# Kernel optimization log

Hardware: AMD Instinct MI355X
Metric: run time of the kernel (lower is better)

## Reference

```python
import jax, jax.numpy as jnp
import numpy as np

DIM = 192
HEADS = 6
HD = 56            # inverted head dim: int((DIM//HEADS) * 1.75)
WIN = 7
N = WIN * WIN      # 49 tokens per window
NW = 64            # windows per image (56x56 map, 7x7 windows)
B_ = 2048          # num_windows * batch
SCALE = (DIM // HEADS) ** (-0.5)  # scale uses ORIGINAL head_dim=32


def _rel_index():
    # same construction as the torch buffer relative_position_index
    coords = np.stack(np.meshgrid(np.arange(WIN), np.arange(WIN), indexing='ij'))
    flat = coords.reshape(2, -1)                      # (2, N)
    rel = flat[:, :, None] - flat[:, None, :]          # (2, N, N)
    rel = rel.transpose(1, 2, 0).astype(np.int64)      # (N, N, 2)
    rel[..., 0] += WIN - 1
    rel[..., 1] += WIN - 1
    rel[..., 0] *= 2 * WIN - 1
    return jnp.asarray(rel.sum(-1), dtype=jnp.int32)   # (N, N)


def setup_inputs() -> dict:
    key = jax.random.key(0)
    ks = jax.random.split(key, 6)
    qkv_out = HEADS * HD * 3  # 1008
    return {
        'x': jax.random.normal(ks[0], (B_, N, DIM), jnp.float32),
        'mask': jnp.zeros((NW, N, N), jnp.float32),
        'qkv_w': (jax.random.normal(ks[1], (DIM, qkv_out), jnp.float32) * 0.02),
        'qkv_b': jnp.zeros((qkv_out,), jnp.float32),
        'rel_bias_table': (jax.random.normal(ks[2], ((2 * WIN - 1) ** 2, HEADS), jnp.float32) * 0.02),
        'rel_index': _rel_index(),
        'lepe_w': (jax.random.normal(ks[3], (HEADS * HD, 1, 3, 3), jnp.float32) * 0.02),
        'lepe_b': jnp.zeros((HEADS * HD,), jnp.float32),
        'proj_w': (jax.random.normal(ks[4], (HEADS * HD, DIM), jnp.float32) * 0.02),
        'proj_b': jnp.zeros((DIM,), jnp.float32),
    }


def reference(x, mask, qkv_w, qkv_b, rel_bias_table, rel_index, lepe_w, lepe_b, proj_w, proj_b):
    B, n, C = x.shape
    # qkv projection: (B, N, 3*H*HD) -> (B, H, N, 3*HD)
    qkv = (x @ qkv_w + qkv_b).reshape(B, n, HEADS, 3 * HD).transpose(0, 2, 1, 3)
    q, k, v = qkv[..., :HD], qkv[..., HD:2 * HD], qkv[..., 2 * HD:]

    v_img = v.transpose(0, 1, 3, 2).reshape(B, HEADS * HD, WIN, WIN)
    lepe = jax.lax.conv_general_dilated(
        v_img, lepe_w, window_strides=(1, 1), padding='SAME',
        dimension_numbers=('NCHW', 'OIHW', 'NCHW'),
        feature_group_count=HEADS * HD) + lepe_b[None, :, None, None]
    lepe = lepe.reshape(B, HEADS * HD, n).transpose(0, 2, 1)  # (B, N, H*HD)

    # attention scores + relative position bias + mask
    attn = jnp.einsum('bhnd,bhmd->bhnm', q * SCALE, k)
    bias = rel_bias_table[rel_index.reshape(-1)].reshape(n, n, HEADS).transpose(2, 0, 1)
    attn = attn + bias[None]
    nW = mask.shape[0]
    attn = attn.reshape(B // nW, nW, HEADS, n, n) + mask[None, :, None]
    attn = jax.nn.softmax(attn.reshape(B, HEADS, n, n), axis=-1)

    out = jnp.einsum('bhnm,bhmd->bhnd', attn, v)
    out = out.transpose(0, 2, 1, 3).reshape(B, n, HEADS * HD) + lepe
    return out @ proj_w + proj_b
```

## Files before the change

kernel.cpp:

```cpp
#include <hip/hip_runtime.h>
#include <hip/hip_bf16.h>

typedef __bf16 bf16x8 __attribute__((ext_vector_type(8)));
typedef unsigned short u16x8 __attribute__((ext_vector_type(8)));
typedef float f32x4 __attribute__((ext_vector_type(4)));

#define NTOK 49
#define NH   6
#define HDIM 56
#define DIMC 192
#define SCALE 0.17677669529663687f

#define WS_QKVWT   0u
#define WS_PROJWT  387072u
#define WS_QKVBS   522240u
#define WS_BMALLT  526272u
#define WS_LEPET   3672000u
#define WS_QKV     3684288u
#define WS_NEED    (WS_QKV + (size_t)100352 * 2016 + 4096)
#define WS_XBF     (WS_QKV + (size_t)100352 * 2016)
#define WS_NEED2   (WS_XBF + (size_t)100352 * 384 + 4096)
#define FB_QKVWT  0
#define FB_PROJWT 387072
#define FB_BIAS6  534528

__device__ __forceinline__ unsigned swzaddr(unsigned base, int row, int colb, int strideb) {
  return base + (unsigned)((row * strideb + colb) ^ ((row & 7) << 4));
}

__device__ __forceinline__ unsigned short f2bu(float f) {
  __hip_bfloat16 h = __float2bfloat16(f);
  unsigned short u;
  __builtin_memcpy(&u, &h, 2);
  return u;
}

__device__ __forceinline__ float bu2f(unsigned short u) {
  union { unsigned int i; float f; } x;
  x.i = ((unsigned int)u) << 16;
  return x.f;
}


__global__ void prep_main(const float* __restrict__ qkv_w,
                          const float* __restrict__ qkv_b,
                          const float* __restrict__ proj_w,
                          const float* __restrict__ tbl,
                          const int* __restrict__ ridx,
                          const float* __restrict__ mask,
                          const float* __restrict__ lepe_w,
                          unsigned char* __restrict__ ws) {
  __hip_bfloat16* qkvwt   = (__hip_bfloat16*)(ws + WS_QKVWT);
  __hip_bfloat16* projwt2 = (__hip_bfloat16*)(ws + WS_PROJWT);
  float*          qkvbs   = (float*)(ws + WS_QKVBS);
  __hip_bfloat16* bmallT  = (__hip_bfloat16*)(ws + WS_BMALLT);
  float*          lepeT   = (float*)(ws + WS_LEPET);
  int idx = blockIdx.x * 256 + threadIdx.x;
  const int n1 = 1008 * 192;
  const int n2 = 192 * 352;
  const int n3 = 1008;
  const int n4 = 64 * 6 * 64 * 64;
  const int n5 = 9 * 336;
  if (idx < n1) {
    int c = idx / 192, k = idx - c * 192;
    float v = qkv_w[k * 1008 + c];
    if (c % 168 < 56) v *= SCALE;
    qkvwt[idx] = __float2bfloat16(v);
  } else if (idx < n1 + n2) {
    int j = idx - n1;
    int n = j / 352, kk = j - n * 352;
    projwt2[j] = __float2bfloat16(kk < 336 ? proj_w[kk * 192 + n] : 0.0f);
  } else if (idx < n1 + n2 + n3) {
    int c = idx - n1 - n2;
    float v = qkv_b[c];
    if (c % 168 < 56) v *= SCALE;
    qkvbs[c] = v;
  } else if (idx < n1 + n2 + n3 + n4) {
    int j = idx - n1 - n2 - n3;
    int wh = j >> 12;
    int e = j & 4095;
    int n = e >> 6, m = e & 63;
    int wdx = wh / 6, h = wh - wdx * 6;
    float v;
    if (n >= NTOK) v = -1e30f;
    else if (m >= NTOK) v = 0.0f;
    else v = tbl[ridx[m * NTOK + n] * NH + h] + mask[wdx * (NTOK * NTOK) + m * NTOK + n];
    bmallT[j] = __float2bfloat16(v);
  } else if (idx < n1 + n2 + n3 + n4 + n5) {
    int j = idx - n1 - n2 - n3 - n4;
    int tap = j / 336, hd = j - tap * 336;
    lepeT[j] = lepe_w[hd * 9 + tap];
  }
}

__global__ __launch_bounds__(256) void xcvt(const float* __restrict__ x,
                                            unsigned char* __restrict__ ws) {
  unsigned char* xbf = ws + WS_XBF;
  int i = blockIdx.x * 256 + threadIdx.x;
  if (i >= 2408448) return;
  const float4* p = (const float4*)(x + (size_t)i * 8);
  float4 a = p[0], b = p[1];
  union { unsigned short u[8]; uint4 q; } pk;
  pk.u[0] = f2bu(a.x); pk.u[1] = f2bu(a.y); pk.u[2] = f2bu(a.z); pk.u[3] = f2bu(a.w);
  pk.u[4] = f2bu(b.x); pk.u[5] = f2bu(b.y); pk.u[6] = f2bu(b.z); pk.u[7] = f2bu(b.w);
  *(uint4*)(xbf + (size_t)i * 16) = pk.q;
}

__global__ __launch_bounds__(256, 2) void qkv_gemm3(unsigned char* __restrict__ ws) {
  __shared__ uint4 smem4[2304];
  unsigned char* sm = (unsigned char*)smem4;
  const __hip_bfloat16* qkvwt = (const __hip_bfloat16*)(ws + WS_QKVWT);
  const float* qkvbs = (const float*)(ws + WS_QKVBS);
  const unsigned char* xbf = ws + WS_XBF;
  unsigned char* qkvbuf = ws + WS_QKV;

  const int tid = threadIdx.x;
  const int lane = tid & 63, wv = tid >> 6;
  const int l15 = lane & 15, l4 = lane >> 4;
  const int b = blockIdx.x;
  const int j = (b & 7) * 1372 + (b >> 3);
  const int nbase = (j % 7) * 144;
  const int mbase = (j / 7) * 64;

  f32x4 acc[9];
#pragma unroll
  for (int nt = 0; nt < 9; ++nt) {
    float bb = qkvbs[nbase + nt * 16 + l15];
    acc[nt] = (f32x4){bb, bb, bb, bb};
  }
  const unsigned char* xrow = xbf + (size_t)(mbase + wv * 16 + l15) * 384;

#pragma unroll
  for (int kh = 0; kh < 2; ++kh) {
    if (kh) __syncthreads();
    for (int jj = tid; jj < 1728; jj += 256) {
      int row = jj / 12, c16 = jj - row * 12;
      uint4 v = *(const uint4*)((const unsigned char*)qkvwt +
                                (size_t)(nbase + row) * 384 + kh * 192 + c16 * 16);
      *(uint4*)(sm + swzaddr(0, row, c16 * 16, 256)) = v;
    }
    bf16x8 afr[3];
#pragma unroll
    for (int kt2 = 0; kt2 < 3; ++kt2)
      afr[kt2] = *(const bf16x8*)(xrow + (kh * 3 + kt2) * 64 + l4 * 16);
    __syncthreads();
#pragma unroll
    for (int kt2 = 0; kt2 < 3; ++kt2) {
#pragma unroll
      for (int nt = 0; nt < 9; ++nt) {
        bf16x8 bf = *(const bf16x8*)(sm + swzaddr(0, nt * 16 + l15, kt2 * 64 + l4 * 16, 256));
        acc[nt] = __builtin_amdgcn_mfma_f32_16x16x32_bf16(afr[kt2], bf, acc[nt], 0, 0, 0);
      }
    }
  }
  __syncthreads();

#pragma unroll
  for (int nt = 0; nt < 9; ++nt)
#pragma unroll
    for (int r = 0; r < 4; ++r) {
      int row = wv * 16 + l4 * 4 + r;
      *(unsigned short*)(sm + swzaddr(0, row, (nt * 16 + l15) * 2, 320)) = f2bu(acc[nt][r]);
    }
  __syncthreads();
  for (int jj = tid; jj < 1152; jj += 256) {
    int row = jj / 18, c16 = jj - row * 18;
    uint4 v = *(const uint4*)(sm + swzaddr(0, row, c16 * 16, 320));
    *(uint4*)(qkvbuf + (size_t)(mbase + row) * 2016 + nbase * 2 + c16 * 16) = v;
  }
}

__global__ __launch_bounds__(256, 2) void qkv_gemm(
    const float* __restrict__ x, unsigned char* __restrict__ ws) {
  __shared__ uint4 smem4[2560];
  unsigned char* sm = (unsigned char*)smem4;
  const __hip_bfloat16* qkvwt = (const __hip_bfloat16*)(ws + WS_QKVWT);
  const float* qkvbs = (const float*)(ws + WS_QKVBS);
  unsigned char* qkvbuf = ws + WS_QKV;

  const int tid = threadIdx.x;
  const int lane = tid & 63, wv = tid >> 6;
  const int l15 = lane & 15, l4 = lane >> 4;
  const int b = blockIdx.x;
  const int j = (b & 7) * 686 + (b >> 3);
  const int nbase = (j % 7) * 144;
  const int mbase = (j / 7) * 128;

  bf16x8 afr[2][6];
#pragma unroll
  for (int mt = 0; mt < 2; ++mt) {
    int g = mbase + wv * 32 + mt * 16 + l15;
    const float* xr = x + (size_t)g * DIMC;
#pragma unroll
    for (int kt = 0; kt < 6; ++kt) {
      const float4* p = (const float4*)(xr + kt * 32 + l4 * 8);
      float4 a = p[0], bb = p[1];
      union { unsigned short u[8]; bf16x8 v; } pk;
      pk.u[0] = f2bu(a.x); pk.u[1] = f2bu(a.y); pk.u[2] = f2bu(a.z); pk.u[3] = f2bu(a.w);
      pk.u[4] = f2bu(bb.x); pk.u[5] = f2bu(bb.y); pk.u[6] = f2bu(bb.z); pk.u[7] = f2bu(bb.w);
      afr[mt][kt] = pk.v;
    }
  }

  f32x4 acc[2][9];
#pragma unroll
  for (int nt = 0; nt < 9; ++nt) {
    float bb = qkvbs[nbase + nt * 16 + l15];
    acc[0][nt] = (f32x4){bb, bb, bb, bb};
    acc[1][nt] = (f32x4){bb, bb, bb, bb};
  }

#pragma unroll
  for (int kh = 0; kh < 2; ++kh) {
    if (kh) __syncthreads();
    for (int jj = tid; jj < 1728; jj += 256) {
      int row = jj / 12, c16 = jj - row * 12;
      uint4 v = *(const uint4*)((const unsigned char*)qkvwt +
                                (size_t)(nbase + row) * 384 + kh * 192 + c16 * 16);
      *(uint4*)(sm + swzaddr(0, row, c16 * 16, 256)) = v;
    }
    __syncthreads();
#pragma unroll
    for (int kt2 = 0; kt2 < 3; ++kt2) {
      const int kt = kh * 3 + kt2;
#pragma unroll
      for (int nt = 0; nt < 9; ++nt) {
        bf16x8 bf = *(const bf16x8*)(sm + swzaddr(0, nt * 16 + l15, kt2 * 64 + l4 * 16, 256));
        acc[0][nt] = __builtin_amdgcn_mfma_f32_16x16x32_bf16(afr[0][kt], bf, acc[0][nt], 0, 0, 0);
        acc[1][nt] = __builtin_amdgcn_mfma_f32_16x16x32_bf16(afr[1][kt], bf, acc[1][nt], 0, 0, 0);
      }
    }
  }
  __syncthreads();

#pragma unroll
  for (int mt = 0; mt < 2; ++mt)
#pragma unroll
    for (int nt = 0; nt < 9; ++nt)
#pragma unroll
      for (int r = 0; r < 4; ++r) {
        int row = wv * 32 + mt * 16 + l4 * 4 + r;
        *(unsigned short*)(sm + swzaddr(0, row, (nt * 16 + l15) * 2, 320)) =
            f2bu(acc[mt][nt][r]);
      }
  __syncthreads();
  for (int jj = tid; jj < 2304; jj += 256) {
    int row = jj / 18, c16 = jj - row * 18;
    uint4 v = *(const uint4*)(sm + swzaddr(0, row, c16 * 16, 320));
    *(uint4*)(qkvbuf + (size_t)(mbase + row) * 2016 + nbase * 2 + c16 * 16) = v;
  }
}

#define A_KS   0u
#define A_VT   8192u
#define A_BMT  16384u
#define A_ATT  24576u
#define A_VS   32768u
#define A_SMEM 40960u

__global__ __launch_bounds__(256, 4) void attn_head(
    const float* __restrict__ lepe_b, unsigned char* __restrict__ ws) {
  __shared__ uint4 smem4[A_SMEM / 16];
  unsigned char* sm = (unsigned char*)smem4;
  const unsigned char* bmallT = ws + WS_BMALLT;
  const float* lepeT = (const float*)(ws + WS_LEPET);
  unsigned char* qkvbuf = ws + WS_QKV;

  const int tid = threadIdx.x;
  const int lane = tid & 63, wv = tid >> 6;
  const int l15 = lane & 15, l4 = lane >> 4;
  const int b = blockIdx.x;
  const int j = (b & 7) * 1536 + (b >> 3);
  const int h = j % 6;
  const int win = j / 6;
  const int wdx = win & 63;
  unsigned char* qbase = qkvbuf + (size_t)win * (NTOK * 2016);

  {
    uint4 z = {0u, 0u, 0u, 0u};
    for (int i = tid; i < 1024; i += 256) smem4[i] = z;
  }
  __syncthreads();

  for (int jj = tid; jj < 343; jj += 256) {
    int m = jj % 49, c = jj / 49;
    const unsigned char* row = qbase + (size_t)m * 2016 + h * 336;
    uint4 kv = *(const uint4*)(row + 112 + c * 16);
    *(uint4*)(sm + swzaddr(A_KS, m, c * 16, 128)) = kv;
    uint4 vv = *(const uint4*)(row + 224 + c * 16);
    *(uint4*)(sm + swzaddr(A_VS, m, c * 16, 128)) = vv;
    union { uint4 q; unsigned short u[8]; } pk; pk.q = vv;
#pragma unroll
    for (int e = 0; e < 8; ++e)
      *(unsigned short*)(sm + swzaddr(A_VT, c * 8 + e, m * 2, 128)) = pk.u[e];
  }
  {
    const uint4* src = (const uint4*)(bmallT + (size_t)(wdx * NH + h) * 8192);
    for (int jj = tid; jj < 512; jj += 256) {
      int n = jj >> 3, c = jj & 7;
      *(uint4*)(sm + swzaddr(A_BMT, n, c * 16, 128)) = src[jj];
    }
  }
  const int arow = wv * 16 + l15;
  const int xr = arow < NTOK ? arow : NTOK - 1;
  bf16x8 qa[2];
#pragma unroll
  for (int kt = 0; kt < 2; ++kt)
    qa[kt] = *(const bf16x8*)(qbase + (size_t)xr * 2016 + h * 336 + kt * 64 + l4 * 16);
  __syncthreads();

  const int mc0 = wv * 16 + l4 * 4;
  f32x4 sv[4];
#pragma unroll
  for (int nt = 0; nt < 4; ++nt) {
    int n = nt * 16 + l15;
    unsigned long long bm8 =
        *(const unsigned long long*)(sm + swzaddr(A_BMT, n, mc0 * 2, 128));
#pragma unroll
    for (int r = 0; r < 4; ++r)
      sv[nt][r] = bu2f((unsigned short)(bm8 >> (16 * r)));
#pragma unroll
    for (int kt = 0; kt < 2; ++kt) {
      bf16x8 kb = *(const bf16x8*)(sm + swzaddr(A_KS, n, kt * 64 + l4 * 16, 128));
      sv[nt] = __builtin_amdgcn_mfma_f32_16x16x32_bf16(qa[kt], kb, sv[nt], 0, 0, 0);
    }
  }

#pragma unroll
  for (int r = 0; r < 4; ++r) {
    float mx = fmaxf(fmaxf(sv[0][r], sv[1][r]), fmaxf(sv[2][r], sv[3][r]));
    mx = fmaxf(mx, __shfl_xor(mx, 1));
    mx = fmaxf(mx, __shfl_xor(mx, 2));
    mx = fmaxf(mx, __shfl_xor(mx, 4));
    mx = fmaxf(mx, __shfl_xor(mx, 8));
    float p0 = __expf(sv[0][r] - mx), p1 = __expf(sv[1][r] - mx);
    float p2 = __expf(sv[2][r] - mx), p3 = __expf(sv[3][r] - mx);
    float sum = p0 + p1 + p2 + p3;
    sum += __shfl_xor(sum, 1);
    sum += __shfl_xor(sum, 2);
    sum += __shfl_xor(sum, 4);
    sum += __shfl_xor(sum, 8);
    float rinv = 1.0f / sum;
    sv[0][r] = p0 * rinv; sv[1][r] = p1 * rinv; sv[2][r] = p2 * rinv; sv[3][r] = p3 * rinv;
  }
#pragma unroll
  for (int nt = 0; nt < 4; ++nt) {
    int n = nt * 16 + l15;
#pragma unroll
    for (int r = 0; r < 4; ++r) {
      int m = mc0 + r;
      if (m < NTOK)
        *(__hip_bfloat16*)(sm + swzaddr(A_ATT, m, n * 2, 128)) = __float2bfloat16(sv[nt][r]);
    }
  }

  bf16x8 pa[2];
#pragma unroll
  for (int kt = 0; kt < 2; ++kt)
    pa[kt] = *(const bf16x8*)(sm + swzaddr(A_ATT, arow, kt * 64 + l4 * 16, 128));
  f32x4 ov[4];
#pragma unroll
  for (int nt = 0; nt < 4; ++nt) {
    f32x4 a0 = (f32x4){0.f, 0.f, 0.f, 0.f};
#pragma unroll
    for (int kt = 0; kt < 2; ++kt) {
      bf16x8 vb = *(const bf16x8*)(sm + swzaddr(A_VT, nt * 16 + l15, kt * 64 + l4 * 16, 128));
      a0 = __builtin_amdgcn_mfma_f32_16x16x32_bf16(pa[kt], vb, a0, 0, 0, 0);
    }
    ov[nt] = a0;
  }

  __syncthreads();
#pragma unroll
  for (int nt = 0; nt < 4; ++nt) {
    int d = nt * 16 + l15;
#pragma unroll
    for (int r = 0; r < 4; ++r) {
      int m = mc0 + r;
      *(float*)(sm + swzaddr(0, m, d * 4, 256)) = ov[nt][r];
    }
  }
  __syncthreads();

  for (int jj = tid; jj < 343; jj += 256) {
    int m = jj % 49, c = jj / 49;
    int y = m / 7, x0 = m - y * 7;
    float4 o0 = *(const float4*)(sm + swzaddr(0, m, c * 32, 256));
    float4 o1 = *(const float4*)(sm + swzaddr(0, m, c * 32 + 16, 256));
    const float4* lb = (const float4*)(lepe_b + h * HDIM + c * 8);
    float4 b0 = lb[0], b1 = lb[1];
    float4 a0, a1;
    a0.x = o0.x + b0.x; a0.y = o0.y + b0.y; a0.z = o0.z + b0.z; a0.w = o0.w + b0.w;
    a1.x = o1.x + b1.x; a1.y = o1.y + b1.y; a1.z = o1.z + b1.z; a1.w = o1.w + b1.w;
#pragma unroll
    for (int dy = 0; dy < 3; ++dy) {
      int yy = y + dy - 1;
      if (yy < 0 || yy >= 7) continue;
#pragma unroll
      for (int dx = 0; dx < 3; ++dx) {
        int xx = x0 + dx - 1;
        if (xx < 0 || xx >= 7) continue;
        int mp = yy * 7 + xx;
        u16x8 vsv = *(const u16x8*)(sm + swzaddr(A_VS, mp, c * 16, 128));
        const float4* wr = (const float4*)(lepeT + (dy * 3 + dx) * 336 + h * HDIM + c * 8);
        float4 w0 = wr[0], w1 = wr[1];
        a0.x += w0.x * bu2f(vsv[0]); a0.y += w0.y * bu2f(vsv[1]);
        a0.z += w0.z * bu2f(vsv[2]); a0.w += w0.w * bu2f(vsv[3]);
        a1.x += w1.x * bu2f(vsv[4]); a1.y += w1.y * bu2f(vsv[5]);
        a1.z += w1.z * bu2f(vsv[6]); a1.w += w1.w * bu2f(vsv[7]);
      }
    }
    union { unsigned short u[8]; uint4 q; } st;
    st.u[0] = f2bu(a0.x); st.u[1] = f2bu(a0.y); st.u[2] = f2bu(a0.z); st.u[3] = f2bu(a0.w);
    st.u[4] = f2bu(a1.x); st.u[5] = f2bu(a1.y); st.u[6] = f2bu(a1.z); st.u[7] = f2bu(a1.w);
    *(uint4*)(qbase + (size_t)m * 2016 + h * 336 + c * 16) = st.q;
  }
}

__global__ __launch_bounds__(256, 3) void proj_gemm(
    const float* __restrict__ proj_b, unsigned char* __restrict__ ws,
    float* __restrict__ out) {
  __shared__ uint4 smem4[2816];
  unsigned char* sm = (unsigned char*)smem4;
  const unsigned char* projwt2 = ws + WS_PROJWT;
  const unsigned char* qkvbuf = ws + WS_QKV;

  const int tid = threadIdx.x;
  const int lane = tid & 63, wv = tid >> 6;
  const int l15 = lane & 15, l4 = lane >> 4;
  const int b = blockIdx.x;
  const int j = (b & 7) * 294 + (b >> 3);
  const int nbase = (j % 3) * 64;
  const int mbase = (j / 3) * 128;

  for (int jj = tid; jj < 2816; jj += 256) {
    int n = jj / 44, c = jj - n * 44;
    uint4 v = *(const uint4*)(projwt2 + (size_t)(nbase + n) * 704 + c * 16);
    *(uint4*)(sm + swzaddr(0, n, c * 16, 704)) = v;
  }
  f32x4 acc[2][4];
#pragma unroll
  for (int nt = 0; nt < 4; ++nt) {
    float bb = proj_b[nbase + nt * 16 + l15];
    acc[0][nt] = (f32x4){bb, bb, bb, bb};
    acc[1][nt] = (f32x4){bb, bb, bb, bb};
  }
  __syncthreads();

  for (int kt = 0; kt < 11; ++kt) {
    int ks = kt * 32 + l4 * 8;
    int hh = ks / 56;
    int rem = ks - hh * 56;
    unsigned aoff = (unsigned)(hh * 336 + rem * 2);
    bf16x8 af[2];
#pragma unroll
    for (int mt = 0; mt < 2; ++mt) {
      int row = mbase + wv * 32 + mt * 16 + l15;
      af[mt] = *(const bf16x8*)(qkvbuf + (size_t)row * 2016 + aoff);
    }
#pragma unroll
    for (int nt = 0; nt < 4; ++nt) {
      bf16x8 pb = *(const bf16x8*)(sm + swzaddr(0, nt * 16 + l15, (kt * 32 + l4 * 8) * 2, 704));
      acc[0][nt] = __builtin_amdgcn_mfma_f32_16x16x32_bf16(af[0], pb, acc[0][nt], 0, 0, 0);
      acc[1][nt] = __builtin_amdgcn_mfma_f32_16x16x32_bf16(af[1], pb, acc[1][nt], 0, 0, 0);
    }
  }
  __syncthreads();

#pragma unroll
  for (int mt = 0; mt < 2; ++mt)
#pragma unroll
    for (int nt = 0; nt < 4; ++nt)
#pragma unroll
      for (int r = 0; r < 4; ++r) {
        int m = wv * 32 + mt * 16 + l4 * 4 + r;
        *(float*)(sm + swzaddr(0, m, (nt * 16 + l15) * 4, 256)) = acc[mt][nt][r];
      }
  __syncthreads();
  for (int jj = tid; jj < 2048; jj += 256) {
    int row = jj >> 4, c = jj & 15;
    uint4 v = *(const uint4*)(sm + swzaddr(0, row, c * 16, 256));
    *(uint4*)((unsigned char*)out + (size_t)(mbase + row) * 768 + nbase * 4 + c * 16) = v;
  }
}


__global__ void prep_fb(const float* __restrict__ qkv_w,
                        const float* __restrict__ proj_w,
                        const float* __restrict__ tbl,
                        const int* __restrict__ ridx,
                        unsigned char* __restrict__ ws) {
  __hip_bfloat16* qkvwt  = (__hip_bfloat16*)(ws + FB_QKVWT);
  __hip_bfloat16* projwt = (__hip_bfloat16*)(ws + FB_PROJWT);
  float* bias6 = (float*)(ws + FB_BIAS6);
  int idx = blockIdx.x * 256 + threadIdx.x;
  const int n1 = 1008 * 192;
  const int n2 = 192 * 384;
  const int n3 = 6 * 49 * 49;
  if (idx < n1) {
    int c = idx / 192, k = idx - c * 192;
    qkvwt[idx] = __float2bfloat16(qkv_w[k * 1008 + c]);
  } else if (idx < n1 + n2) {
    int j = idx - n1;
    int c = j / 384, kk = j - c * 384;
    projwt[j] = __float2bfloat16(kk < 336 ? proj_w[kk * 192 + c] : 0.0f);
  } else if (idx < n1 + n2 + n3) {
    int j = idx - n1 - n2;
    int h = j / 2401, mn = j - h * 2401;
    bias6[j] = tbl[ridx[mn] * 6 + h];
  }
}

#define QS_OFF  0
#define KS_OFF  8192
#define VT_OFF  16384
#define ATT_OFF 24576
#define SMEM_BYTES 32768

__global__ __launch_bounds__(256, 4) void winattn_fb(
    const float* __restrict__ x, const float* __restrict__ mask,
    const float* __restrict__ qkv_b, const float* __restrict__ lepe_w,
    const float* __restrict__ lepe_b, const float* __restrict__ proj_b,
    const unsigned char* __restrict__ ws, float* __restrict__ out) {
  __shared__ uint4 smem4[SMEM_BYTES / 16];
  unsigned char* sm = (unsigned char*)smem4;
  const __hip_bfloat16* qkvwt  = (const __hip_bfloat16*)(ws + FB_QKVWT);
  const __hip_bfloat16* projwt = (const __hip_bfloat16*)(ws + FB_PROJWT);
  const float* bias6 = (const float*)(ws + FB_BIAS6);

  const int tid = threadIdx.x;
  const int lane = tid & 63, wv = tid >> 6;
  const int l15 = lane & 15, l4 = lane >> 4;
  const int blk = blockIdx.x;
  const int wdx = blk & 63;
  {
    uint4 z = {0u, 0u, 0u, 0u};
    for (int i = tid; i < SMEM_BYTES / 16; i += 256) smem4[i] = z;
  }
  const int arow = wv * 16 + l15;
  const float* xg = x + (size_t)blk * (NTOK * DIMC);
  const int xr = arow < NTOK ? arow : NTOK - 1;
  bf16x8 afr[6];
#pragma unroll
  for (int kt = 0; kt < 6; ++kt) {
    const float4* p = (const float4*)(xg + xr * DIMC + kt * 32 + l4 * 8);
    float4 a = p[0], b = p[1];
    union { unsigned short u[8]; bf16x8 v; } pk;
    pk.u[0] = f2bu(a.x); pk.u[1] = f2bu(a.y); pk.u[2] = f2bu(a.z); pk.u[3] = f2bu(a.w);
    pk.u[4] = f2bu(b.x); pk.u[5] = f2bu(b.y); pk.u[6] = f2bu(b.z); pk.u[7] = f2bu(b.w);
    afr[kt] = pk.v;
  }
  f32x4 pacc[12];
#pragma unroll
  for (int nt = 0; nt < 12; ++nt) {
    float pb = proj_b[nt * 16 + l15];
    pacc[nt] = (f32x4){pb, pb, pb, pb};
  }
  const float* maskw = mask + wdx * (NTOK * NTOK);
  __syncthreads();

  for (int h = 0; h < NH; ++h) {
    for (int i = tid; i < NTOK * NTOK; i += 256) {
      int row = i / NTOK, col = i - row * NTOK;
      *(unsigned short*)(sm + ATT_OFF + row * 128 + col * 2) =
          f2bu(bias6[h * (NTOK * NTOK) + i] + maskw[i]);
    }
#pragma unroll
    for (int nt = 0; nt < 11; ++nt) {
      int cl = nt * 16 + l15;
      int cg = h * 168 + cl; if (cg > 1007) cg = 1007;
      float bias = qkv_b[cg];
      f32x4 acc = (f32x4){bias, bias, bias, bias};
#pragma unroll
      for (int kt = 0; kt < 6; ++kt) {
        bf16x8 bf = *(const bf16x8*)(qkvwt + cg * DIMC + kt * 32 + l4 * 8);
        acc = __builtin_amdgcn_mfma_f32_16x16x32_bf16(afr[kt], bf, acc, 0, 0, 0);
      }
      if (cl < 168) {
#pragma unroll
        for (int r = 0; r < 4; ++r) {
          int m = wv * 16 + l4 * 4 + r;
          if (m < NTOK) {
            float vv = acc[r];
            if (cl < 56)
              *(__hip_bfloat16*)(sm + swzaddr(QS_OFF, m, cl * 2, 128)) = __float2bfloat16(vv);
            else if (cl < 112)
              *(__hip_bfloat16*)(sm + swzaddr(KS_OFF, m, (cl - 56) * 2, 128)) = __float2bfloat16(vv);
            else
              *(__hip_bfloat16*)(sm + swzaddr(VT_OFF, cl - 112, m * 2, 128)) = __float2bfloat16(vv);
          }
        }
      }
    }
    __syncthreads();
    bf16x8 qa[2];
#pragma unroll
    for (int kt = 0; kt < 2; ++kt)
      qa[kt] = *(const bf16x8*)(sm + swzaddr(QS_OFF, arow, (kt * 32 + l4 * 8) * 2, 128));
    f32x4 sv[4];
#pragma unroll
    for (int nt = 0; nt < 4; ++nt) {
      f32x4 acc = (f32x4){0.f, 0.f, 0.f, 0.f};
#pragma unroll
      for (int kt = 0; kt < 2; ++kt) {
        bf16x8 kb = *(const bf16x8*)(sm + swzaddr(KS_OFF, nt * 16 + l15, (kt * 32 + l4 * 8) * 2, 128));
        acc = __builtin_amdgcn_mfma_f32_16x16x32_bf16(qa[kt], kb, acc, 0, 0, 0);
      }
      sv[nt] = acc;
    }
#pragma unroll
    for (int nt = 0; nt < 4; ++nt) {
      int n = nt * 16 + l15;
#pragma unroll
      for (int r = 0; r < 4; ++r) {
        int m = wv * 16 + l4 * 4 + r;
        int mc = m < NTOK ? m : NTOK - 1;
        float vv;
        if (n < NTOK) {
          float add = __bfloat162float(
              *(const __hip_bfloat16*)(sm + ATT_OFF + mc * 128 + n * 2));
          vv = SCALE * sv[nt][r] + add;
        } else {
          vv = -1e30f;
        }
        sv[nt][r] = vv;
      }
    }
#pragma unroll
    for (int r = 0; r < 4; ++r) {
      float mx = fmaxf(fmaxf(sv[0][r], sv[1][r]), fmaxf(sv[2][r], sv[3][r]));
      mx = fmaxf(mx, __shfl_xor(mx, 1));
      mx = fmaxf(mx, __shfl_xor(mx, 2));
      mx = fmaxf(mx, __shfl_xor(mx, 4));
      mx = fmaxf(mx, __shfl_xor(mx, 8));
      float p0 = __expf(sv[0][r] - mx), p1 = __expf(sv[1][r] - mx);
      float p2 = __expf(sv[2][r] - mx), p3 = __expf(sv[3][r] - mx);
      float sum = p0 + p1 + p2 + p3;
      sum += __shfl_xor(sum, 1);
      sum += __shfl_xor(sum, 2);
      sum += __shfl_xor(sum, 4);
      sum += __shfl_xor(sum, 8);
      float rinv = 1.0f / sum;
      sv[0][r] = p0 * rinv; sv[1][r] = p1 * rinv; sv[2][r] = p2 * rinv; sv[3][r] = p3 * rinv;
    }
#pragma unroll
    for (int nt = 0; nt < 4; ++nt) {
      int n = nt * 16 + l15;
#pragma unroll
      for (int r = 0; r < 4; ++r) {
        int m = wv * 16 + l4 * 4 + r;
        if (m < NTOK)
          *(__hip_bfloat16*)(sm + swzaddr(ATT_OFF, m, n * 2, 128)) = __float2bfloat16(sv[nt][r]);
      }
    }
    bf16x8 pa[2];
#pragma unroll
    for (int kt = 0; kt < 2; ++kt)
      pa[kt] = *(const bf16x8*)(sm + swzaddr(ATT_OFF, arow, (kt * 32 + l4 * 8) * 2, 128));
    f32x4 ov[4];
#pragma unroll
    for (int nt = 0; nt < 4; ++nt) {
      f32x4 acc = (f32x4){0.f, 0.f, 0.f, 0.f};
#pragma unroll
      for (int kt = 0; kt < 2; ++kt) {
        bf16x8 vb = *(const bf16x8*)(sm + swzaddr(VT_OFF, nt * 16 + l15, (kt * 32 + l4 * 8) * 2, 128));
        acc = __builtin_amdgcn_mfma_f32_16x16x32_bf16(pa[kt], vb, acc, 0, 0, 0);
      }
      ov[nt] = acc;
    }
#pragma unroll
    for (int nt = 0; nt < 4; ++nt) {
      int d = nt * 16 + l15;
      if (d < HDIM) {
        const float* lw = lepe_w + (h * HDIM + d) * 9;
        float w9[9];
#pragma unroll
        for (int t9 = 0; t9 < 9; ++t9) w9[t9] = lw[t9];
        float lb = lepe_b[h * HDIM + d];
#pragma unroll
        for (int r = 0; r < 4; ++r) {
          int m = wv * 16 + l4 * 4 + r;
          if (m < NTOK) {
            int y = m / 7, x0 = m - y * 7;
            float lac = lb;
#pragma unroll
            for (int dy = 0; dy < 3; ++dy)
#pragma unroll
              for (int dx = 0; dx < 3; ++dx) {
                int yy = y + dy - 1, xx = x0 + dx - 1;
                if (yy >= 0 && yy < 7 && xx >= 0 && xx < 7) {
                  float vvv = __bfloat162float(
                      *(const __hip_bfloat16*)(sm + swzaddr(VT_OFF, d, (yy * 7 + xx) * 2, 128)));
                  lac += w9[dy * 3 + dx] * vvv;
                }
              }
            *(__hip_bfloat16*)(sm + swzaddr(QS_OFF, m, d * 2, 128)) =
                __float2bfloat16(ov[nt][r] + lac);
          }
        }
      }
    }
    bf16x8 oa[2];
#pragma unroll
    for (int kt = 0; kt < 2; ++kt)
      oa[kt] = *(const bf16x8*)(sm + swzaddr(QS_OFF, arow, (kt * 32 + l4 * 8) * 2, 128));
#pragma unroll
    for (int nt = 0; nt < 12; ++nt) {
#pragma unroll
      for (int kt = 0; kt < 2; ++kt) {
        bf16x8 pb = *(const bf16x8*)(projwt + (nt * 16 + l15) * 384 + h * HDIM + kt * 32 + l4 * 8);
        pacc[nt] = __builtin_amdgcn_mfma_f32_16x16x32_bf16(oa[kt], pb, pacc[nt], 0, 0, 0);
      }
    }
    __syncthreads();
  }
  float* og = out + (size_t)blk * (NTOK * DIMC);
#pragma unroll
  for (int nt = 0; nt < 12; ++nt) {
#pragma unroll
    for (int r = 0; r < 4; ++r) {
      int m = wv * 16 + l4 * 4 + r;
      if (m < NTOK) og[m * DIMC + nt * 16 + l15] = pacc[nt][r];
    }
  }
}


extern "C" void kernel_launch(void* const* d_in, const int* in_sizes, int n_in,
                              void* d_out, int out_size, void* d_ws, size_t ws_size,
                              hipStream_t stream) {
  const float* x      = (const float*)d_in[0];
  const float* mask   = (const float*)d_in[1];
  const float* qkv_w  = (const float*)d_in[2];
  const float* qkv_b  = (const float*)d_in[3];
  const float* tbl    = (const float*)d_in[4];
  const int*   ridx   = (const int*)d_in[5];
  const float* lepe_w = (const float*)d_in[6];
  const float* lepe_b = (const float*)d_in[7];
  const float* proj_w = (const float*)d_in[8];
  const float* proj_b = (const float*)d_in[9];
  unsigned char* ws = (unsigned char*)d_ws;
  float* out = (float*)d_out;

  if (ws_size >= WS_NEED) {
    const int n_prep = 1008 * 192 + 192 * 352 + 1008 + 64 * 6 * 64 * 64 + 9 * 336;
    prep_main<<<dim3((n_prep + 255) / 256), dim3(256), 0, stream>>>(
        qkv_w, qkv_b, proj_w, tbl, ridx, mask, lepe_w, ws);
    if (ws_size >= WS_NEED2) {
      xcvt<<<dim3(9408), dim3(256), 0, stream>>>(x, ws);
      qkv_gemm3<<<dim3(10976), dim3(256), 0, stream>>>(ws);
    } else {
      qkv_gemm<<<dim3(5488), dim3(256), 0, stream>>>(x, ws);
    }
    attn_head<<<dim3(12288), dim3(256), 0, stream>>>(lepe_b, ws);
    proj_gemm<<<dim3(2352), dim3(256), 0, stream>>>(proj_b, ws, out);
  } else {
    prep_fb<<<dim3(1101), dim3(256), 0, stream>>>(qkv_w, proj_w, tbl, ridx, ws);
    winattn_fb<<<dim3(2048), dim3(256), 0, stream>>>(x, mask, qkv_b, lepe_w, lepe_b,
                                                     proj_b, ws, out);
  }
}
```

Baseline: 296.3 us.

## Shrink attn_head LDS footprint, load bias to registers, store V as fp32

The bias/mask tile is now read straight from global memory into registers, and Q is loaded before the LDS zero-fill so both loads are in flight early. The attention-probability tile now reuses the K region after an added barrier, so the separate bias and prob LDS regions go away. LDS per block drops from 40 KB to 32 KB, which may allow more resident blocks. V for LePE is converted to fp32 once at staging so the 3x3 conv avoids repeated bf16 unpacking, at the cost of twice the LDS bytes per V read. It also uses a hardware reciprocal for the softmax normaliser.

```diff
diff --git a/kernel.cpp b/kernel.cpp
--- a/kernel.cpp
+++ b/kernel.cpp
@@ -253,10 +253,8 @@
 
 #define A_KS   0u
 #define A_VT   8192u
-#define A_BMT  16384u
-#define A_ATT  24576u
-#define A_VS   32768u
-#define A_SMEM 40960u
+#define A_VS   16384u
+#define A_SMEM 32768u
 
 __global__ __launch_bounds__(256, 4) void attn_head(
     const float* __restrict__ lepe_b, unsigned char* __restrict__ ws) {
@@ -276,6 +274,22 @@
   const int wdx = win & 63;
   unsigned char* qbase = qkvbuf + (size_t)win * (NTOK * 2016);
 
+  const int arow = wv * 16 + l15;
+  const int xr = arow < NTOK ? arow : NTOK - 1;
+  const int mc0 = wv * 16 + l4 * 4;
+
+  bf16x8 qa[2];
+#pragma unroll
+  for (int kt = 0; kt < 2; ++kt)
+    qa[kt] = *(const bf16x8*)(qbase + (size_t)xr * 2016 + h * 336 + kt * 64 + l4 * 16);
+  unsigned long long bm8[4];
+  {
+    const unsigned char* bmrow = bmallT + (size_t)(wdx * NH + h) * 8192;
+#pragma unroll
+    for (int nt = 0; nt < 4; ++nt)
+      bm8[nt] = *(const unsigned long long*)(bmrow + (nt * 16 + l15) * 128 + mc0 * 2);
+  }
+
   {
     uint4 z = {0u, 0u, 0u, 0u};
     for (int i = tid; i < 1024; i += 256) smem4[i] = z;
@@ -288,37 +302,25 @@
     uint4 kv = *(const uint4*)(row + 112 + c * 16);
     *(uint4*)(sm + swzaddr(A_KS, m, c * 16, 128)) = kv;
     uint4 vv = *(const uint4*)(row + 224 + c * 16);
-    *(uint4*)(sm + swzaddr(A_VS, m, c * 16, 128)) = vv;
     union { uint4 q; unsigned short u[8]; } pk; pk.q = vv;
 #pragma unroll
     for (int e = 0; e < 8; ++e)
       *(unsigned short*)(sm + swzaddr(A_VT, c * 8 + e, m * 2, 128)) = pk.u[e];
-  }
-  {
-    const uint4* src = (const uint4*)(bmallT + (size_t)(wdx * NH + h) * 8192);
-    for (int jj = tid; jj < 512; jj += 256) {
-      int n = jj >> 3, c = jj & 7;
-      *(uint4*)(sm + swzaddr(A_BMT, n, c * 16, 128)) = src[jj];
-    }
-  }
-  const int arow = wv * 16 + l15;
-  const int xr = arow < NTOK ? arow : NTOK - 1;
-  bf16x8 qa[2];
-#pragma unroll
-  for (int kt = 0; kt < 2; ++kt)
-    qa[kt] = *(const bf16x8*)(qbase + (size_t)xr * 2016 + h * 336 + kt * 64 + l4 * 16);
-  __syncthreads();
-
-  const int mc0 = wv * 16 + l4 * 4;
+    float4 vf0, vf1;
+    vf0.x = bu2f(pk.u[0]); vf0.y = bu2f(pk.u[1]); vf0.z = bu2f(pk.u[2]); vf0.w = bu2f(pk.u[3]);
+    vf1.x = bu2f(pk.u[4]); vf1.y = bu2f(pk.u[5]); vf1.z = bu2f(pk.u[6]); vf1.w = bu2f(pk.u[7]);
+    *(float4*)(sm + swzaddr(A_VS, m, c * 32, 256)) = vf0;
+    *(float4*)(sm + swzaddr(A_VS, m, c * 32 + 16, 256)) = vf1;
+  }
+  __syncthreads();
+
   f32x4 sv[4];
 #pragma unroll
   for (int nt = 0; nt < 4; ++nt) {
+#pragma unroll
+    for (int r = 0; r < 4; ++r)
+      sv[nt][r] = bu2f((unsigned short)(bm8[nt] >> (16 * r)));
     int n = nt * 16 + l15;
-    unsigned long long bm8 =
-        *(const unsigned long long*)(sm + swzaddr(A_BMT, n, mc0 * 2, 128));
-#pragma unroll
-    for (int r = 0; r < 4; ++r)
-      sv[nt][r] = bu2f((unsigned short)(bm8 >> (16 * r)));
 #pragma unroll
     for (int kt = 0; kt < 2; ++kt) {
       bf16x8 kb = *(const bf16x8*)(sm + swzaddr(A_KS, n, kt * 64 + l4 * 16, 128));
@@ -340,9 +342,11 @@
     sum += __shfl_xor(sum, 2);
     sum += __shfl_xor(sum, 4);
     sum += __shfl_xor(sum, 8);
-    float rinv = 1.0f / sum;
+    float rinv = __builtin_amdgcn_rcpf(sum);
     sv[0][r] = p0 * rinv; sv[1][r] = p1 * rinv; sv[2][r] = p2 * rinv; sv[3][r] = p3 * rinv;
   }
+
+  __syncthreads();
 #pragma unroll
   for (int nt = 0; nt < 4; ++nt) {
     int n = nt * 16 + l15;
@@ -350,14 +354,14 @@
     for (int r = 0; r < 4; ++r) {
       int m = mc0 + r;
       if (m < NTOK)
-        *(__hip_bfloat16*)(sm + swzaddr(A_ATT, m, n * 2, 128)) = __float2bfloat16(sv[nt][r]);
+        *(__hip_bfloat16*)(sm + swzaddr(A_KS, m, n * 2, 128)) = __float2bfloat16(sv[nt][r]);
     }
   }
 
   bf16x8 pa[2];
 #pragma unroll
   for (int kt = 0; kt < 2; ++kt)
-    pa[kt] = *(const bf16x8*)(sm + swzaddr(A_ATT, arow, kt * 64 + l4 * 16, 128));
+    pa[kt] = *(const bf16x8*)(sm + swzaddr(A_KS, arow, kt * 64 + l4 * 16, 128));
   f32x4 ov[4];
 #pragma unroll
   for (int nt = 0; nt < 4; ++nt) {
@@ -385,13 +389,12 @@
   for (int jj = tid; jj < 343; jj += 256) {
     int m = jj % 49, c = jj / 49;
     int y = m / 7, x0 = m - y * 7;
-    float4 o0 = *(const float4*)(sm + swzaddr(0, m, c * 32, 256));
-    float4 o1 = *(const float4*)(sm + swzaddr(0, m, c * 32 + 16, 256));
+    float4 a0 = *(const float4*)(sm + swzaddr(0, m, c * 32, 256));
+    float4 a1 = *(const float4*)(sm + swzaddr(0, m, c * 32 + 16, 256));
     const float4* lb = (const float4*)(lepe_b + h * HDIM + c * 8);
     float4 b0 = lb[0], b1 = lb[1];
-    float4 a0, a1;
-    a0.x = o0.x + b0.x; a0.y = o0.y + b0.y; a0.z = o0.z + b0.z; a0.w = o0.w + b0.w;
-    a1.x = o1.x + b1.x; a1.y = o1.y + b1.y; a1.z = o1.z + b1.z; a1.w = o1.w + b1.w;
+    a0.x += b0.x; a0.y += b0.y; a0.z += b0.z; a0.w += b0.w;
+    a1.x += b1.x; a1.y += b1.y; a1.z += b1.z; a1.w += b1.w;
 #pragma unroll
     for (int dy = 0; dy < 3; ++dy) {
       int yy = y + dy - 1;
@@ -401,13 +404,12 @@
         int xx = x0 + dx - 1;
         if (xx < 0 || xx >= 7) continue;
         int mp = yy * 7 + xx;
-        u16x8 vsv = *(const u16x8*)(sm + swzaddr(A_VS, mp, c * 16, 128));
+        float4 v0 = *(const float4*)(sm + swzaddr(A_VS, mp, c * 32, 256));
+        float4 v1 = *(const float4*)(sm + swzaddr(A_VS, mp, c * 32 + 16, 256));
         const float4* wr = (const float4*)(lepeT + (dy * 3 + dx) * 336 + h * HDIM + c * 8);
         float4 w0 = wr[0], w1 = wr[1];
-        a0.x += w0.x * bu2f(vsv[0]); a0.y += w0.y * bu2f(vsv[1]);
-        a0.z += w0.z * bu2f(vsv[2]); a0.w += w0.w * bu2f(vsv[3]);
-        a1.x += w1.x * bu2f(vsv[4]); a1.y += w1.y * bu2f(vsv[5]);
-        a1.z += w1.z * bu2f(vsv[6]); a1.w += w1.w * bu2f(vsv[7]);
+        a0.x += w0.x * v0.x; a0.y += w0.y * v0.y; a0.z += w0.z * v0.z; a0.w += w0.w * v0.w;
+        a1.x += w1.x * v1.x; a1.y += w1.y * v1.y; a1.z += w1.z * v1.z; a1.w += w1.w * v1.w;
       }
     }
     union { unsigned short u[8]; uint4 q; } st;
```

Result: no change. 291.8 us (-1.5%).
